# Kernel optimization log

Measured on AMD Instinct MI355X. Metric: run time of the kernel, lower is better.

Reference implementation:

```python
import jax, jax.numpy as jnp
import numpy as np

PRIOR_HOURS = 48.0
INIT_TIME = 0.0
K = 13  # nr_ref_time_points (time_space)
L = 200  # time steps (axis_2)
D = 64   # features (axis_3)
B = 64

REF_TIME = jnp.asarray(np.linspace(INIT_TIME, PRIOR_HOURS, K).reshape(K, 1, 1), dtype=jnp.float32)


def setup_inputs() -> dict:
    key = jax.random.key(0)
    ks = jax.random.split(key, 9)
    X = jax.random.normal(ks[0], (B, L, D), dtype=jnp.float32)
    T = jax.random.uniform(ks[1], (B, L, D), dtype=jnp.float32) * PRIOR_HOURS
    M = (jax.random.uniform(ks[2], (B, L, D)) > 0.5).astype(jnp.float32)
    DT = jax.random.uniform(ks[3], (B, L, D), dtype=jnp.float32)
    # trainable weights (keras random_normal initializer, stddev=0.05)
    alpha = jax.random.normal(ks[4], (K, 1, 1), dtype=jnp.float32) * 0.05
    w_v = jax.random.normal(ks[5], (K, L, D), dtype=jnp.float32) * 0.05
    w_t = jax.random.normal(ks[6], (K, L, D, 4), dtype=jnp.float32) * 0.05
    b_v = jax.random.normal(ks[7], (K, 1, D), dtype=jnp.float32) * 0.05
    b_t = jax.random.normal(ks[8], (K, L, D, 1), dtype=jnp.float32) * 0.05
    return {"X": X, "T": T, "M": M, "DT": DT, "alpha": alpha,
            "w_v": w_v, "w_t": w_t, "b_v": b_v, "b_t": b_t}


def reference(X, T, M, DT, alpha, w_v, w_t, b_v, b_t):
    # broadcast inputs over the K reference time points: [B,1,L,D] -> [B,K,L,D]
    dist = jnp.abs(T[:, None, :, :] - REF_TIME)                 # [B,K,L,D]
    kernel = jnp.exp(-jax.nn.relu(alpha) * dist)                # [B,K,L,D]
    intensity = jax.nn.relu(X[:, None, :, :] * kernel)          # [B,K,L,D]
    shp = intensity.shape
    x = jnp.broadcast_to(X[:, None, :, :], shp)
    dt = jnp.broadcast_to(DT[:, None, :, :], shp)
    m = jnp.broadcast_to(M[:, None, :, :], shp)
    feat = jnp.stack([x, dt, intensity, m], axis=-1)            # [B,K,L,D,4]
    # stage 1: weighted reduce over the 4-feature axis (b_t broadcasts over it)
    lat = jax.nn.relu(jnp.sum(w_t * feat + b_t, axis=-1))       # [B,K,L,D]
    # stage 2: weighted reduce over the time-step axis L (b_v broadcasts over it)
    out = jax.nn.relu(jnp.sum(w_v * lat + b_v, axis=2))         # [B,K,D]
    return out
```

## Files before the change

### kernel.cpp

```cpp
#include <hip/hip_runtime.h>


#define NB 64
#define NK 13
#define NL 200
#define ND 64

__global__ __launch_bounds__(256) void alnn_fused(
    const float* __restrict__ X, const float* __restrict__ T,
    const float* __restrict__ M, const float* __restrict__ DT,
    const float* __restrict__ alpha, const float* __restrict__ w_v,
    const float* __restrict__ w_t, const float* __restrict__ b_v,
    const float* __restrict__ b_t, float* __restrict__ out)
{
    const int k   = blockIdx.x >> 5;
    const int bp  = blockIdx.x & 31;
    const int tid = threadIdx.x;
    const int dq  = tid & 15;
    const int d0  = dq << 2;
    const int lsub = tid >> 4;

    const float a    = fmaxf(alpha[k], 0.0f);
    const float reft = 4.0f * (float)k;

    const float4* X4  = (const float4*)X;
    const float4* T4  = (const float4*)T;
    const float4* M4  = (const float4*)M;
    const float4* DT4 = (const float4*)DT;
    const float4* WT4 = (const float4*)w_t;
    const float4* BT4 = (const float4*)b_t;
    const float4* WV4 = (const float4*)w_v;

    const int b0 = bp << 1;
    const int b1 = b0 + 1;

    float4 acc0 = make_float4(0.f, 0.f, 0.f, 0.f);
    float4 acc1 = make_float4(0.f, 0.f, 0.f, 0.f);

#define COMP(c, wt, acc) {                                                \
        const float dist  = fabsf(t4.c - reft);                           \
        const float kern  = __expf(-a * dist);                            \
        const float inten = fmaxf(x4.c * kern, 0.0f);                     \
        const float sf = wt.x * x4.c + wt.y * dt4.c + wt.z * inten +      \
                         wt.w * m4.c + 4.0f * bt4.c;                      \
        acc.c = fmaf(wv4.c, fmaxf(sf, 0.0f), acc.c);                      \
    }

    #pragma unroll 2
    for (int j = 0; j < 13; ++j) {
        const int l = (j << 4) + lsub;
        if (l < NL) {
            const int wd = (k * NL + l) * ND + d0;
            const float4 wtA = WT4[wd + 0];
            const float4 wtB = WT4[wd + 1];
            const float4 wtC = WT4[wd + 2];
            const float4 wtD = WT4[wd + 3];
            const float4 bt4 = BT4[wd >> 2];
            const float4 wv4 = WV4[wd >> 2];
            {
                const int io = ((b0 * NL + l) * ND + d0) >> 2;
                const float4 x4  = X4[io];
                const float4 t4  = T4[io];
                const float4 m4  = M4[io];
                const float4 dt4 = DT4[io];
                COMP(x, wtA, acc0) COMP(y, wtB, acc0)
                COMP(z, wtC, acc0) COMP(w, wtD, acc0)
            }
            {
                const int io = ((b1 * NL + l) * ND + d0) >> 2;
                const float4 x4  = X4[io];
                const float4 t4  = T4[io];
                const float4 m4  = M4[io];
                const float4 dt4 = DT4[io];
                COMP(x, wtA, acc1) COMP(y, wtB, acc1)
                COMP(z, wtC, acc1) COMP(w, wtD, acc1)
            }
        }
    }
#undef COMP

    __shared__ float4 red[16][2][16];
    red[lsub][0][dq] = acc0;
    red[lsub][1][dq] = acc1;
    __syncthreads();

    if (tid < 128) {
        const int b = tid >> 6;
        const int d = tid & 63;
        const float* redf = (const float*)red;
        float s = 0.0f;
        #pragma unroll
        for (int ls = 0; ls < 16; ++ls)
            s += redf[ls * 128 + b * 64 + d];
        const int bi = b0 + b;
        s += (float)NL * b_v[k * ND + d];
        out[(bi * NK + k) * ND + d] = fmaxf(s, 0.0f);
    }
}

extern "C" void kernel_launch(void* const* d_in, const int* in_sizes, int n_in,
                              void* d_out, int out_size, void* d_ws, size_t ws_size,
                              hipStream_t stream) {
    const float* X     = (const float*)d_in[0];
    const float* T     = (const float*)d_in[1];
    const float* M     = (const float*)d_in[2];
    const float* DT    = (const float*)d_in[3];
    const float* alpha = (const float*)d_in[4];
    const float* w_v   = (const float*)d_in[5];
    const float* w_t   = (const float*)d_in[6];
    const float* b_v   = (const float*)d_in[7];
    const float* b_t   = (const float*)d_in[8];
    float* out = (float*)d_out;

    alnn_fused<<<NK * 32, 256, 0, stream>>>(X, T, M, DT, alpha, w_v, w_t, b_v, b_t, out);
}
```

Measured before the change: 93.47 us.

## Split into two-stage L-chunked partial reduction with inputs reused across all K

Changes the work split so each block handles a chunk of 4 time steps for 8 batches and loops over all 13 reference points. Each X/T/M/DT element is then loaded once instead of once per K. Blocks are assigned L-chunks with an XCD-aware remap, and partial sums over L go to a workspace. A second kernel reduces the 50 chunks and applies bias and relu. This adds a second launch, workspace traffic, and 13 float4 accumulators per thread, which raises register pressure.

```diff
diff --git a/kernel.cpp b/kernel.cpp
--- a/kernel.cpp
+++ b/kernel.cpp
@@ -5,23 +5,33 @@
 #define NK 13
 #define NL 200
 #define ND 64
+#define ND4 16
+#define GB 8
+#define LC 4
+#define NC (NL / LC)
 
-__global__ __launch_bounds__(256) void alnn_fused(
+__global__ __launch_bounds__(256) void alnn_stage1(
     const float* __restrict__ X, const float* __restrict__ T,
     const float* __restrict__ M, const float* __restrict__ DT,
     const float* __restrict__ alpha, const float* __restrict__ w_v,
-    const float* __restrict__ w_t, const float* __restrict__ b_v,
-    const float* __restrict__ b_t, float* __restrict__ out)
+    const float* __restrict__ w_t, const float* __restrict__ b_t,
+    float4* __restrict__ part)
 {
-    const int k   = blockIdx.x >> 5;
-    const int bp  = blockIdx.x & 31;
+    const int bid = blockIdx.x;
+    const int xcd = bid & 7;
+    const int j   = bid >> 3;
+    const int c   = ((j >> 3) << 3) | xcd;
+    if (c >= NC) return;
+    const int bg  = j & 7;
+
     const int tid = threadIdx.x;
     const int dq  = tid & 15;
+    const int s   = tid >> 4;
+    const int bb  = s >> 1;
+    const int lh  = s & 1;
+    const int b   = (bg << 3) + bb;
+    const int la  = c * LC + (lh << 1);
     const int d0  = dq << 2;
-    const int lsub = tid >> 4;
-
-    const float a    = fmaxf(alpha[k], 0.0f);
-    const float reft = 4.0f * (float)k;
 
     const float4* X4  = (const float4*)X;
     const float4* T4  = (const float4*)T;
@@ -31,71 +41,96 @@
     const float4* BT4 = (const float4*)b_t;
     const float4* WV4 = (const float4*)w_v;
 
-    const int b0 = bp << 1;
-    const int b1 = b0 + 1;
+    const int io0 = (b * NL + la) * ND4 + dq;
+    const int io1 = io0 + ND4;
+    const float4 xA = X4[io0],  xB = X4[io1];
+    const float4 tA = T4[io0],  tB = T4[io1];
+    const float4 mA = M4[io0],  mB = M4[io1];
+    const float4 dA = DT4[io0], dB = DT4[io1];
 
-    float4 acc0 = make_float4(0.f, 0.f, 0.f, 0.f);
-    float4 acc1 = make_float4(0.f, 0.f, 0.f, 0.f);
+    float4 acc[NK];
+    #pragma unroll
+    for (int k = 0; k < NK; ++k) acc[k] = make_float4(0.f, 0.f, 0.f, 0.f);
 
-#define COMP(c, wt, acc) {                                                \
-        const float dist  = fabsf(t4.c - reft);                           \
-        const float kern  = __expf(-a * dist);                            \
-        const float inten = fmaxf(x4.c * kern, 0.0f);                     \
-        const float sf = wt.x * x4.c + wt.y * dt4.c + wt.z * inten +      \
-                         wt.w * m4.c + 4.0f * bt4.c;                      \
-        acc.c = fmaf(wv4.c, fmaxf(sf, 0.0f), acc.c);                      \
+#define COMP(c_, wt, xv, tv, mv, dv, bt4, wv4, A) {                       \
+        const float dist  = fabsf(tv.c_ - reft);                          \
+        const float inten = fmaxf(xv.c_ * __expf(-a * dist), 0.f);        \
+        const float sf = wt.x * xv.c_ + wt.y * dv.c_ + wt.z * inten +     \
+                         wt.w * mv.c_ + 4.f * bt4.c_;                     \
+        A.c_ = fmaf(wv4.c_, fmaxf(sf, 0.f), A.c_);                        \
     }
 
-    #pragma unroll 2
-    for (int j = 0; j < 13; ++j) {
-        const int l = (j << 4) + lsub;
-        if (l < NL) {
-            const int wd = (k * NL + l) * ND + d0;
-            const float4 wtA = WT4[wd + 0];
-            const float4 wtB = WT4[wd + 1];
-            const float4 wtC = WT4[wd + 2];
-            const float4 wtD = WT4[wd + 3];
-            const float4 bt4 = BT4[wd >> 2];
-            const float4 wv4 = WV4[wd >> 2];
-            {
-                const int io = ((b0 * NL + l) * ND + d0) >> 2;
-                const float4 x4  = X4[io];
-                const float4 t4  = T4[io];
-                const float4 m4  = M4[io];
-                const float4 dt4 = DT4[io];
-                COMP(x, wtA, acc0) COMP(y, wtB, acc0)
-                COMP(z, wtC, acc0) COMP(w, wtD, acc0)
-            }
-            {
-                const int io = ((b1 * NL + l) * ND + d0) >> 2;
-                const float4 x4  = X4[io];
-                const float4 t4  = T4[io];
-                const float4 m4  = M4[io];
-                const float4 dt4 = DT4[io];
-                COMP(x, wtA, acc1) COMP(y, wtB, acc1)
-                COMP(z, wtC, acc1) COMP(w, wtD, acc1)
-            }
+    #pragma unroll
+    for (int k = 0; k < NK; ++k) {
+        const float a    = fmaxf(alpha[k], 0.f);
+        const float reft = 4.f * (float)k;
+        const int wq = (k * NL + la) * ND4 + dq;
+        const int w0 = (k * NL + la) * ND + d0;
+        {
+            const float4 wt0 = WT4[w0 + 0];
+            const float4 wt1 = WT4[w0 + 1];
+            const float4 wt2 = WT4[w0 + 2];
+            const float4 wt3 = WT4[w0 + 3];
+            const float4 bt4 = BT4[wq];
+            const float4 wv4 = WV4[wq];
+            COMP(x, wt0, xA, tA, mA, dA, bt4, wv4, acc[k])
+            COMP(y, wt1, xA, tA, mA, dA, bt4, wv4, acc[k])
+            COMP(z, wt2, xA, tA, mA, dA, bt4, wv4, acc[k])
+            COMP(w, wt3, xA, tA, mA, dA, bt4, wv4, acc[k])
+        }
+        {
+            const float4 wt0 = WT4[w0 + ND + 0];
+            const float4 wt1 = WT4[w0 + ND + 1];
+            const float4 wt2 = WT4[w0 + ND + 2];
+            const float4 wt3 = WT4[w0 + ND + 3];
+            const float4 bt4 = BT4[wq + ND4];
+            const float4 wv4 = WV4[wq + ND4];
+            COMP(x, wt0, xB, tB, mB, dB, bt4, wv4, acc[k])
+            COMP(y, wt1, xB, tB, mB, dB, bt4, wv4, acc[k])
+            COMP(z, wt2, xB, tB, mB, dB, bt4, wv4, acc[k])
+            COMP(w, wt3, xB, tB, mB, dB, bt4, wv4, acc[k])
         }
     }
 #undef COMP
 
-    __shared__ float4 red[16][2][16];
-    red[lsub][0][dq] = acc0;
-    red[lsub][1][dq] = acc1;
-    __syncthreads();
+    #pragma unroll
+    for (int k = 0; k < NK; ++k) {
+        acc[k].x += __shfl_xor(acc[k].x, 16);
+        acc[k].y += __shfl_xor(acc[k].y, 16);
+        acc[k].z += __shfl_xor(acc[k].z, 16);
+        acc[k].w += __shfl_xor(acc[k].w, 16);
+    }
 
-    if (tid < 128) {
-        const int b = tid >> 6;
-        const int d = tid & 63;
-        const float* redf = (const float*)red;
-        float s = 0.0f;
-        #pragma unroll
-        for (int ls = 0; ls < 16; ++ls)
-            s += redf[ls * 128 + b * 64 + d];
-        const int bi = b0 + b;
-        s += (float)NL * b_v[k * ND + d];
-        out[(bi * NK + k) * ND + d] = fmaxf(s, 0.0f);
+    const int pb = ((c * NB + b) * NK) * ND4 + dq;
+    #pragma unroll
+    for (int k = 0; k < NK; ++k) {
+        if ((k < 7) == (lh == 0))
+            part[pb + k * ND4] = acc[k];
     }
+}
+
+__global__ __launch_bounds__(256) void alnn_stage2(
+    const float4* __restrict__ part, const float* __restrict__ b_v,
+    float4* __restrict__ out)
+{
+    const int tid = blockIdx.x * 256 + threadIdx.x;
+    const int dq  = tid & 15;
+    const int bk  = tid >> 4;
+    const int k   = bk % NK;
+
+    float4 s = make_float4(0.f, 0.f, 0.f, 0.f);
+    #pragma unroll 5
+    for (int c = 0; c < NC; ++c) {
+        const float4 p = part[(c * NB * NK + bk) * ND4 + dq];
+        s.x += p.x; s.y += p.y; s.z += p.z; s.w += p.w;
+    }
+    const float4 bv = ((const float4*)b_v)[k * ND4 + dq];
+    float4 r;
+    r.x = fmaxf(s.x + 200.f * bv.x, 0.f);
+    r.y = fmaxf(s.y + 200.f * bv.y, 0.f);
+    r.z = fmaxf(s.z + 200.f * bv.z, 0.f);
+    r.w = fmaxf(s.w + 200.f * bv.w, 0.f);
+    out[tid] = r;
 }
 
 extern "C" void kernel_launch(void* const* d_in, const int* in_sizes, int n_in,
@@ -110,7 +145,9 @@
     const float* w_t   = (const float*)d_in[6];
     const float* b_v   = (const float*)d_in[7];
     const float* b_t   = (const float*)d_in[8];
-    float* out = (float*)d_out;
 
-    alnn_fused<<<NK * 32, 256, 0, stream>>>(X, T, M, DT, alpha, w_v, w_t, b_v, b_t, out);
+    float4* part = (float4*)d_ws;
+
+    alnn_stage1<<<512, 256, 0, stream>>>(X, T, M, DT, alpha, w_v, w_t, b_t, part);
+    alnn_stage2<<<(NB * NK * ND4) / 256, 256, 0, stream>>>(part, b_v, (float4*)d_out);
 }
```

Result: slower. 100.7 us (+7.7%).
